# Performance work log

Hardware: AMD Instinct MI355X
Metric: run time of the kernel (lower is better)

The kernel has to match this reference:

```python
import jax, jax.numpy as jnp
import numpy as np

N_AGENTS = 64
B = 256
D = 256  # hidden_size == comm_dim


def setup_inputs() -> dict:
    key = jax.random.key(0)
    ks = jax.random.split(key, 4)
    s = 1.0 / np.sqrt(D)
    return {
        "hidden_state": jax.random.normal(ks[0], (B * N_AGENTS, D), jnp.float32),
        "W_act": jax.random.normal(ks[1], (D, D), jnp.float32) * s,
        "b_act": jnp.zeros((D,), jnp.float32),
        "W_sum": jax.random.normal(ks[2], (D, D), jnp.float32) * s,
        "b_sum": jnp.zeros((D,), jnp.float32),
        "W_head": jax.random.normal(ks[3], (D, D), jnp.float32) * s,
        "b_head": jnp.zeros((D,), jnp.float32),
    }


def reference(hidden_state, W_act, b_act, W_sum, b_sum, W_head, b_head):
    n = N_AGENTS
    # comm_act linear: (b*n, D)
    comm = hidden_state @ W_act.T + b_act
    b = comm.shape[0] // n
    comm = comm.reshape(b, n, D)
    # comm_mask = ones(n,n) - eye(n); agents all alive, comm_action_one=True
    mask = (jnp.ones((n, n), comm.dtype) - jnp.eye(n, dtype=comm.dtype))
    # original: expand to (b,n,n,D), mask, divide by (n-1), sum over dim=1 (sender i)
    # fused equivalent: out[b,j,d] = sum_i mask[i,j] * comm[b,i,d] / (n-1)
    agg = jnp.einsum('ij,bid->bjd', mask, comm) / (n - 1)
    x = agg.reshape(b * n, D) @ W_sum.T + b_sum      # comm_sum_head
    out = jax.nn.relu(x @ W_head.T + b_head)          # comm_head + active_fun
    return out
```

## Files before the change

kernel.cpp:

```cpp
#include <hip/hip_runtime.h>
#include <hip/hip_bf16.h>

#define DIM 256
#define NAGENT 64
#define NBATCH 256

typedef __bf16 bf16_t;
typedef bf16_t bf16x4 __attribute__((ext_vector_type(4)));
typedef bf16_t bf16x8 __attribute__((ext_vector_type(8)));
typedef float f32x4 __attribute__((ext_vector_type(4)));

__global__ __launch_bounds__(1024) void prep_kernel(
    const float* __restrict__ Wh, const float* __restrict__ Ws,
    const float* __restrict__ Wa, const float* __restrict__ ba,
    const float* __restrict__ bs, const float* __restrict__ bh,
    bf16_t* __restrict__ Wc, float* __restrict__ bcw) {
  const int b = blockIdx.x;
  const int t = threadIdx.x;
  const int jg = t & 63;
  const int kc = t >> 6;

  __shared__ float whl[DIM];
  __shared__ float t1l[DIM];
  __shared__ f32x4 part[16][64];

  if (t < 64) *(f32x4*)&whl[t * 4] = *(const f32x4*)&Wh[b * DIM + t * 4];

  f32x4 wa[16];
#pragma unroll
  for (int ki = 0; ki < 16; ++ki)
    wa[ki] = *(const f32x4*)&Wa[(kc * 16 + ki) * DIM + jg * 4];

  __syncthreads();

  {
    f32x4 a = {0.f, 0.f, 0.f, 0.f};
#pragma unroll
    for (int ki = 0; ki < 16; ++ki) {
      const int k = kc * 16 + ki;
      a += whl[k] * *(const f32x4*)&Ws[k * DIM + jg * 4];
    }
    part[kc][jg] = a;
  }
  __syncthreads();
  if (t < 64) {
    f32x4 s = part[0][t];
#pragma unroll
    for (int r = 1; r < 16; ++r) s += part[r][t];
    *(f32x4*)&t1l[t * 4] = s;
  }
  __syncthreads();

  {
    f32x4 a = {0.f, 0.f, 0.f, 0.f};
#pragma unroll
    for (int ki = 0; ki < 16; ++ki) a += t1l[kc * 16 + ki] * wa[ki];
    part[kc][jg] = a;
  }
  __syncthreads();
  if (t < 64) {
    f32x4 s = part[0][t];
#pragma unroll
    for (int r = 1; r < 16; ++r) s += part[r][t];
    bf16x4 wb;
    wb[0] = (bf16_t)s[0]; wb[1] = (bf16_t)s[1];
    wb[2] = (bf16_t)s[2]; wb[3] = (bf16_t)s[3];
    *(bf16x4*)&Wc[b * DIM + t * 4] = wb;
    const f32x4 t14 = *(const f32x4*)&t1l[t * 4];
    const f32x4 ba4 = *(const f32x4*)&ba[t * 4];
    const f32x4 wh4 = *(const f32x4*)&whl[t * 4];
    const f32x4 bs4 = *(const f32x4*)&bs[t * 4];
    const f32x4 pp = t14 * ba4 + wh4 * bs4;
    float p = pp[0] + pp[1] + pp[2] + pp[3];
#pragma unroll
    for (int s2 = 32; s2 > 0; s2 >>= 1) p += __shfl_down(p, s2, 64);
    if (t == 0) bcw[b] = p + bh[b];
  }
}

__global__ __launch_bounds__(512) void fused_kernel(
    const float* __restrict__ h, const bf16_t* __restrict__ Wc,
    const float* __restrict__ bcw, float* __restrict__ out) {
  const int b = blockIdx.x;
  const int t = threadIdx.x;
  const int cg = t & 63;
  const int rg = t >> 6;

  __shared__ __align__(16) bf16_t g[NAGENT * DIM];
  __shared__ f32x4 ps[8][64];

  const float* hb = h + (size_t)b * NAGENT * DIM;

  f32x4 v[8];
#pragma unroll
  for (int i = 0; i < 8; ++i)
    v[i] = *(const f32x4*)&hb[(rg * 8 + i) * DIM + cg * 4];

  const int lane = t & 63, lrow = lane & 15, lgrp = lane >> 4;
  bf16x8 bfrag[8][2];
#pragma unroll
  for (int kk = 0; kk < 8; ++kk) {
#pragma unroll
    for (int ct = 0; ct < 2; ++ct) {
      const int col = rg * 32 + ct * 16 + lrow;
      bfrag[kk][ct] = *(const bf16x8*)&Wc[col * DIM + kk * 32 + lgrp * 8];
    }
  }
  const float bv0 = bcw[rg * 32 + lrow];
  const float bv1 = bcw[rg * 32 + 16 + lrow];

  f32x4 s4 = v[0];
#pragma unroll
  for (int i = 1; i < 8; ++i) s4 += v[i];
  ps[rg][cg] = s4;
  __syncthreads();
  f32x4 hs = ps[0][cg];
#pragma unroll
  for (int r = 1; r < 8; ++r) hs += ps[r][cg];

  const float inv = 1.0f / 63.0f;
#pragma unroll
  for (int i = 0; i < 8; ++i) {
    const int row = rg * 8 + i;
    const f32x4 gv = (hs - v[i]) * inv;
    bf16x4 gb;
    gb[0] = (bf16_t)gv[0]; gb[1] = (bf16_t)gv[1];
    gb[2] = (bf16_t)gv[2]; gb[3] = (bf16_t)gv[3];
    *(bf16x4*)&g[row * DIM + ((cg * 4) ^ ((row & 7) << 3))] = gb;
  }
  __syncthreads();

  f32x4 acc[4][2];
#pragma unroll
  for (int rt = 0; rt < 4; ++rt)
#pragma unroll
    for (int ct = 0; ct < 2; ++ct) acc[rt][ct] = (f32x4){0.f, 0.f, 0.f, 0.f};

#pragma unroll
  for (int kk = 0; kk < 8; ++kk) {
    const int k0 = kk * 32 + lgrp * 8;
#pragma unroll
    for (int rt = 0; rt < 4; ++rt) {
      const int arow = rt * 16 + lrow;
      const bf16x8 afrag =
          *(const bf16x8*)&g[arow * DIM + (k0 ^ ((arow & 7) << 3))];
      acc[rt][0] = __builtin_amdgcn_mfma_f32_16x16x32_bf16(afrag, bfrag[kk][0], acc[rt][0], 0, 0, 0);
      acc[rt][1] = __builtin_amdgcn_mfma_f32_16x16x32_bf16(afrag, bfrag[kk][1], acc[rt][1], 0, 0, 0);
    }
  }

  float* ob = out + (size_t)b * NAGENT * DIM;
#pragma unroll
  for (int ct = 0; ct < 2; ++ct) {
    const int col = rg * 32 + ct * 16 + lrow;
    const float bcv = ct ? bv1 : bv0;
#pragma unroll
    for (int rt = 0; rt < 4; ++rt) {
#pragma unroll
      for (int r = 0; r < 4; ++r) {
        const int row = rt * 16 + lgrp * 4 + r;
        const float val = acc[rt][ct][r] + bcv;
        ob[row * DIM + col] = val > 0.f ? val : 0.f;
      }
    }
  }
}

extern "C" void kernel_launch(void* const* d_in, const int* in_sizes, int n_in,
                              void* d_out, int out_size, void* d_ws, size_t ws_size,
                              hipStream_t stream) {
  const float* h  = (const float*)d_in[0];
  const float* Wa = (const float*)d_in[1];
  const float* ba = (const float*)d_in[2];
  const float* Ws = (const float*)d_in[3];
  const float* bs = (const float*)d_in[4];
  const float* Wh = (const float*)d_in[5];
  const float* bh = (const float*)d_in[6];
  float* out = (float*)d_out;

  char* ws = (char*)d_ws;
  bf16_t* Wc  = (bf16_t*)ws;
  float*  bcw = (float*)(ws + 128 * 1024);

  prep_kernel<<<NBATCH, 1024, 0, stream>>>(Wh, Ws, Wa, ba, bs, bh, Wc, bcw);
  fused_kernel<<<NBATCH, 512, 0, stream>>>(h, Wc, bcw, out);
}
```

Baseline: 22.85 us.

## Split combined weight into two chained GEMMs instead of triple-product precompute

The prep kernel now folds only W_sum and W_act into one combined matrix and converts W_head to bf16, dropping the second 256x256x256 weight product. The fused kernel then runs two back-to-back MFMA GEMMs per batch, staging the intermediate in a second swizzled LDS buffer with the combined bias added before the head GEMM. This shortens the serial prep work at the cost of doubling the MFMA work and LDS use in the main kernel, plus an extra bf16 rounding of the intermediate, which likely changes accuracy.

```diff
diff --git a/kernel.cpp b/kernel.cpp
--- a/kernel.cpp
+++ b/kernel.cpp
@@ -11,26 +11,20 @@
 typedef float f32x4 __attribute__((ext_vector_type(4)));
 
 __global__ __launch_bounds__(1024) void prep_kernel(
-    const float* __restrict__ Wh, const float* __restrict__ Ws,
-    const float* __restrict__ Wa, const float* __restrict__ ba,
-    const float* __restrict__ bs, const float* __restrict__ bh,
-    bf16_t* __restrict__ Wc, float* __restrict__ bcw) {
+    const float* __restrict__ Ws, const float* __restrict__ Wa,
+    const float* __restrict__ Wh, const float* __restrict__ ba,
+    const float* __restrict__ bs,
+    bf16_t* __restrict__ Wsa, bf16_t* __restrict__ Whbf,
+    float* __restrict__ vvec) {
   const int b = blockIdx.x;
   const int t = threadIdx.x;
   const int jg = t & 63;
   const int kc = t >> 6;
 
-  __shared__ float whl[DIM];
-  __shared__ float t1l[DIM];
+  __shared__ float wsl[DIM];
   __shared__ f32x4 part[16][64];
 
-  if (t < 64) *(f32x4*)&whl[t * 4] = *(const f32x4*)&Wh[b * DIM + t * 4];
-
-  f32x4 wa[16];
-#pragma unroll
-  for (int ki = 0; ki < 16; ++ki)
-    wa[ki] = *(const f32x4*)&Wa[(kc * 16 + ki) * DIM + jg * 4];
-
+  if (t < 64) *(f32x4*)&wsl[t * 4] = *(const f32x4*)&Ws[b * DIM + t * 4];
   __syncthreads();
 
   {
@@ -38,24 +32,17 @@
 #pragma unroll
     for (int ki = 0; ki < 16; ++ki) {
       const int k = kc * 16 + ki;
-      a += whl[k] * *(const f32x4*)&Ws[k * DIM + jg * 4];
+      a += wsl[k] * *(const f32x4*)&Wa[k * DIM + jg * 4];
     }
     part[kc][jg] = a;
   }
-  __syncthreads();
-  if (t < 64) {
-    f32x4 s = part[0][t];
-#pragma unroll
-    for (int r = 1; r < 16; ++r) s += part[r][t];
-    *(f32x4*)&t1l[t * 4] = s;
-  }
-  __syncthreads();
-
-  {
-    f32x4 a = {0.f, 0.f, 0.f, 0.f};
-#pragma unroll
-    for (int ki = 0; ki < 16; ++ki) a += t1l[kc * 16 + ki] * wa[ki];
-    part[kc][jg] = a;
+  if (t >= 64 && t < 128) {
+    const int c = t - 64;
+    const f32x4 w4 = *(const f32x4*)&Wh[b * DIM + c * 4];
+    bf16x4 wb;
+    wb[0] = (bf16_t)w4[0]; wb[1] = (bf16_t)w4[1];
+    wb[2] = (bf16_t)w4[2]; wb[3] = (bf16_t)w4[3];
+    *(bf16x4*)&Whbf[b * DIM + c * 4] = wb;
   }
   __syncthreads();
   if (t < 64) {
@@ -65,29 +52,29 @@
     bf16x4 wb;
     wb[0] = (bf16_t)s[0]; wb[1] = (bf16_t)s[1];
     wb[2] = (bf16_t)s[2]; wb[3] = (bf16_t)s[3];
-    *(bf16x4*)&Wc[b * DIM + t * 4] = wb;
-    const f32x4 t14 = *(const f32x4*)&t1l[t * 4];
+    *(bf16x4*)&Wsa[b * DIM + t * 4] = wb;
+    const f32x4 ws4 = *(const f32x4*)&wsl[t * 4];
     const f32x4 ba4 = *(const f32x4*)&ba[t * 4];
-    const f32x4 wh4 = *(const f32x4*)&whl[t * 4];
-    const f32x4 bs4 = *(const f32x4*)&bs[t * 4];
-    const f32x4 pp = t14 * ba4 + wh4 * bs4;
+    const f32x4 pp = ws4 * ba4;
     float p = pp[0] + pp[1] + pp[2] + pp[3];
 #pragma unroll
     for (int s2 = 32; s2 > 0; s2 >>= 1) p += __shfl_down(p, s2, 64);
-    if (t == 0) bcw[b] = p + bh[b];
+    if (t == 0) vvec[b] = p + bs[b];
   }
 }
 
 __global__ __launch_bounds__(512) void fused_kernel(
-    const float* __restrict__ h, const bf16_t* __restrict__ Wc,
-    const float* __restrict__ bcw, float* __restrict__ out) {
+    const float* __restrict__ h, const bf16_t* __restrict__ Wsa,
+    const bf16_t* __restrict__ Whbf, const float* __restrict__ vvec,
+    const float* __restrict__ bh, float* __restrict__ out) {
   const int b = blockIdx.x;
   const int t = threadIdx.x;
   const int cg = t & 63;
   const int rg = t >> 6;
 
-  __shared__ __align__(16) bf16_t g[NAGENT * DIM];
-  __shared__ f32x4 ps[8][64];
+  __shared__ __align__(16) bf16_t gA[NAGENT * DIM];
+  __shared__ __align__(16) bf16_t gB[NAGENT * DIM];
+  f32x4* ps = (f32x4*)gB;
 
   const float* hb = h + (size_t)b * NAGENT * DIM;
 
@@ -97,26 +84,26 @@
     v[i] = *(const f32x4*)&hb[(rg * 8 + i) * DIM + cg * 4];
 
   const int lane = t & 63, lrow = lane & 15, lgrp = lane >> 4;
-  bf16x8 bfrag[8][2];
-#pragma unroll
-  for (int kk = 0; kk < 8; ++kk) {
-#pragma unroll
-    for (int ct = 0; ct < 2; ++ct) {
-      const int col = rg * 32 + ct * 16 + lrow;
-      bfrag[kk][ct] = *(const bf16x8*)&Wc[col * DIM + kk * 32 + lgrp * 8];
-    }
-  }
-  const float bv0 = bcw[rg * 32 + lrow];
-  const float bv1 = bcw[rg * 32 + 16 + lrow];
+  bf16x8 bf1[8][2];
+#pragma unroll
+  for (int kk = 0; kk < 8; ++kk)
+#pragma unroll
+    for (int ct = 0; ct < 2; ++ct)
+      bf1[kk][ct] = *(const bf16x8*)&Wsa[(rg * 32 + ct * 16 + lrow) * DIM +
+                                         kk * 32 + lgrp * 8];
+  const float vv0 = vvec[rg * 32 + lrow];
+  const float vv1 = vvec[rg * 32 + 16 + lrow];
+  const float bh0 = bh[rg * 32 + lrow];
+  const float bh1 = bh[rg * 32 + 16 + lrow];
 
   f32x4 s4 = v[0];
 #pragma unroll
   for (int i = 1; i < 8; ++i) s4 += v[i];
-  ps[rg][cg] = s4;
-  __syncthreads();
-  f32x4 hs = ps[0][cg];
-#pragma unroll
-  for (int r = 1; r < 8; ++r) hs += ps[r][cg];
+  ps[rg * 64 + cg] = s4;
+  __syncthreads();
+  f32x4 hs = ps[0 * 64 + cg];
+#pragma unroll
+  for (int r = 1; r < 8; ++r) hs += ps[r * 64 + cg];
 
   const float inv = 1.0f / 63.0f;
 #pragma unroll
@@ -126,9 +113,17 @@
     bf16x4 gb;
     gb[0] = (bf16_t)gv[0]; gb[1] = (bf16_t)gv[1];
     gb[2] = (bf16_t)gv[2]; gb[3] = (bf16_t)gv[3];
-    *(bf16x4*)&g[row * DIM + ((cg * 4) ^ ((row & 7) << 3))] = gb;
-  }
-  __syncthreads();
+    *(bf16x4*)&gA[row * DIM + ((cg * 4) ^ ((row & 7) << 3))] = gb;
+  }
+  __syncthreads();
+
+  bf16x8 bf2[8][2];
+#pragma unroll
+  for (int kk = 0; kk < 8; ++kk)
+#pragma unroll
+    for (int ct = 0; ct < 2; ++ct)
+      bf2[kk][ct] = *(const bf16x8*)&Whbf[(rg * 32 + ct * 16 + lrow) * DIM +
+                                          kk * 32 + lgrp * 8];
 
   f32x4 acc[4][2];
 #pragma unroll
@@ -143,26 +138,57 @@
     for (int rt = 0; rt < 4; ++rt) {
       const int arow = rt * 16 + lrow;
       const bf16x8 afrag =
-          *(const bf16x8*)&g[arow * DIM + (k0 ^ ((arow & 7) << 3))];
-      acc[rt][0] = __builtin_amdgcn_mfma_f32_16x16x32_bf16(afrag, bfrag[kk][0], acc[rt][0], 0, 0, 0);
-      acc[rt][1] = __builtin_amdgcn_mfma_f32_16x16x32_bf16(afrag, bfrag[kk][1], acc[rt][1], 0, 0, 0);
+          *(const bf16x8*)&gA[arow * DIM + (k0 ^ ((arow & 7) << 3))];
+      acc[rt][0] = __builtin_amdgcn_mfma_f32_16x16x32_bf16(afrag, bf1[kk][0], acc[rt][0], 0, 0, 0);
+      acc[rt][1] = __builtin_amdgcn_mfma_f32_16x16x32_bf16(afrag, bf1[kk][1], acc[rt][1], 0, 0, 0);
     }
   }
 
-  float* ob = out + (size_t)b * NAGENT * DIM;
 #pragma unroll
   for (int ct = 0; ct < 2; ++ct) {
     const int col = rg * 32 + ct * 16 + lrow;
-    const float bcv = ct ? bv1 : bv0;
-#pragma unroll
-    for (int rt = 0; rt < 4; ++rt) {
+    const float vb = ct ? vv1 : vv0;
+#pragma unroll
+    for (int rt = 0; rt < 4; ++rt)
 #pragma unroll
       for (int r = 0; r < 4; ++r) {
         const int row = rt * 16 + lgrp * 4 + r;
-        const float val = acc[rt][ct][r] + bcv;
+        gB[row * DIM + (col ^ ((row & 7) << 3))] = (bf16_t)(acc[rt][ct][r] + vb);
+      }
+  }
+  __syncthreads();
+
+#pragma unroll
+  for (int rt = 0; rt < 4; ++rt)
+#pragma unroll
+    for (int ct = 0; ct < 2; ++ct) acc[rt][ct] = (f32x4){0.f, 0.f, 0.f, 0.f};
+
+#pragma unroll
+  for (int kk = 0; kk < 8; ++kk) {
+    const int k0 = kk * 32 + lgrp * 8;
+#pragma unroll
+    for (int rt = 0; rt < 4; ++rt) {
+      const int arow = rt * 16 + lrow;
+      const bf16x8 afrag =
+          *(const bf16x8*)&gB[arow * DIM + (k0 ^ ((arow & 7) << 3))];
+      acc[rt][0] = __builtin_amdgcn_mfma_f32_16x16x32_bf16(afrag, bf2[kk][0], acc[rt][0], 0, 0, 0);
+      acc[rt][1] = __builtin_amdgcn_mfma_f32_16x16x32_bf16(afrag, bf2[kk][1], acc[rt][1], 0, 0, 0);
+    }
+  }
+
+  float* ob = out + (size_t)b * NAGENT * DIM;
+#pragma unroll
+  for (int ct = 0; ct < 2; ++ct) {
+    const int col = rg * 32 + ct * 16 + lrow;
+    const float bb = ct ? bh1 : bh0;
+#pragma unroll
+    for (int rt = 0; rt < 4; ++rt)
+#pragma unroll
+      for (int r = 0; r < 4; ++r) {
+        const int row = rt * 16 + lgrp * 4 + r;
+        const float val = acc[rt][ct][r] + bb;
         ob[row * DIM + col] = val > 0.f ? val : 0.f;
       }
-    }
   }
 }
 
@@ -179,9 +205,10 @@
   float* out = (float*)d_out;
 
   char* ws = (char*)d_ws;
-  bf16_t* Wc  = (bf16_t*)ws;
-  float*  bcw = (float*)(ws + 128 * 1024);
-
-  prep_kernel<<<NBATCH, 1024, 0, stream>>>(Wh, Ws, Wa, ba, bs, bh, Wc, bcw);
-  fused_kernel<<<NBATCH, 512, 0, stream>>>(h, Wc, bcw, out);
+  bf16_t* Wsa  = (bf16_t*)ws;
+  bf16_t* Whbf = (bf16_t*)(ws + 128 * 1024);
+  float*  vvec = (float*)(ws + 256 * 1024);
+
+  prep_kernel<<<NBATCH, 1024, 0, stream>>>(Ws, Wa, Wh, ba, bs, Wsa, Whbf, vvec);
+  fused_kernel<<<NBATCH, 512, 0, stream>>>(h, Wsa, Whbf, vvec, bh, out);
 }
```

After: 24.46 us. 1.07x slower.
